# Kernel optimization log

Measured on AMD Instinct MI355X. Metric: run time of the kernel, lower is better.

Reference implementation:

```python
import jax, jax.numpy as jnp
import numpy as np

LAMBDA_SOFTMAX = 10.0  # opt.lambda_softmax
LEAKY_SLOPE = 0.1


def l2norm(x, axis):
    # matches torch F.normalize(p=2, eps=1e-12)
    n = jnp.linalg.norm(x, axis=axis, keepdims=True)
    return x / jnp.clip(n, 1e-12)


def setup_inputs() -> dict:
    key = jax.random.key(0)
    k1, k2, k3, k4, k5 = jax.random.split(key, 5)
    I, Q, T, S, D = 64, 49, 64, 64, 256  # n_img, n_region, n_txt, max_words, feature_size
    return {
        "local_img_query": jax.random.normal(k1, (I, Q, D), jnp.float32),
        "local_img_value": jax.random.normal(k2, (I, Q, D), jnp.float32),
        "local_text_key": jax.random.normal(k3, (T, S, D), jnp.float32),
        "local_text_value": jax.random.normal(k4, (T, S, D), jnp.float32),
        "text_length": jax.random.randint(k5, (T,), 8, S + 1, jnp.int32),
    }


def reference(local_img_query, local_img_value, local_text_key, local_text_value, text_length):
    # Vectorized form of the per-sentence Python loop in compute_i2t_sim.
    # Variable sentence lengths are handled with a mask over the padded word axis,
    # which reproduces the ragged torch math exactly (see comments).
    T, S, D = local_text_key.shape
    I, Q, _ = local_img_query.shape

    qn = l2norm(local_img_query, -1)   # [I,Q,D]
    kn = l2norm(local_text_key, -1)    # [T,S,D]

    # bmm(txt_key_norm, queryT): (B,S,D)x(B,D,Q) -> here [T,I,S,Q]
    attn = jnp.einsum('tsd,iqd->tisq', kn, qn)
    attn = jnp.where(attn > 0, attn, LEAKY_SLOPE * attn)      # LeakyReLU(0.1)
    # l2norm(attn, 2) normalizes over queryL per (t,i,s) row -> independent of padding
    attn = l2norm(attn, -1)
    attn = jnp.swapaxes(attn, 2, 3)                            # [T,I,Q,S]

    mask = jnp.arange(S)[None, :] < text_length[:, None]       # [T,S]
    logits = jnp.where(mask[:, None, None, :], attn * LAMBDA_SOFTMAX, -jnp.inf)
    attn = jax.nn.softmax(logits, axis=-1)                     # padded words -> exactly 0

    # focal_equal with sourceL = actual n_word of each sentence
    n_word = text_length.astype(attn.dtype)[:, None, None, None]
    funcF = attn * n_word - jnp.sum(attn, axis=-1, keepdims=True)
    fattn = (funcF > 0).astype(attn.dtype)                     # padded attn=0 -> funcF<0 -> 0
    tmp = fattn * attn
    attn = tmp / jnp.sum(tmp, axis=-1, keepdims=True)

    # bmm(valueT, attnT) -> weighted text context per (txt, img): [T,I,Q,D]
    wei = jnp.einsum('tsd,tiqs->tiqd', local_text_value, attn)
    wei = l2norm(wei, -1)

    # cosine similarity with image values along d, then mean over regions
    v = local_img_value[None]                                  # [1,I,Q,D]
    w12 = jnp.sum(v * wei, -1)
    denom = jnp.linalg.norm(v, axis=-1) * jnp.linalg.norm(wei, axis=-1)
    sim = w12 / jnp.clip(denom, 1e-8)                          # [T,I,Q]
    i2t = sim.mean(axis=-1)                                    # [T,I]
    return i2t.T                                               # [n_img, n_txt]
```

## Files before the change

kernel.cpp:

```cpp
#include <hip/hip_runtime.h>
#include <math.h>

#define I_N 64
#define Q_N 49
#define T_N 64
#define S_N 64
#define D_N 256

typedef __attribute__((ext_vector_type(8))) short short8;
typedef __attribute__((ext_vector_type(4))) float f32x4;
typedef unsigned short ushort_t;

__device__ __forceinline__ float waveReduceSum64(float v) {
    v += __shfl_xor(v, 1);
    v += __shfl_xor(v, 2);
    v += __shfl_xor(v, 4);
    v += __shfl_xor(v, 8);
    v += __shfl_xor(v, 16);
    v += __shfl_xor(v, 32);
    return v;
}

__device__ __forceinline__ ushort_t f2bf(float x) {
    unsigned u = __builtin_bit_cast(unsigned, x);
    unsigned r = (u + 0x7fffu + ((u >> 16) & 1u)) >> 16;
    return (ushort_t)r;
}
__device__ __forceinline__ float bf2f(ushort_t h) {
    unsigned u = ((unsigned)h) << 16;
    return __builtin_bit_cast(float, u);
}
__device__ __forceinline__ void split_bf16(float x, ushort_t& h, ushort_t& l) {
    h = f2bf(x);
    l = f2bf(x - bf2f(h));
}

__global__ void prep_norm(const float* __restrict__ q_in, const float* __restrict__ v_in,
                          const float* __restrict__ k_in,
                          ushort_t* __restrict__ qfh, ushort_t* __restrict__ qfl,
                          ushort_t* __restrict__ kfh, ushort_t* __restrict__ kfl,
                          float* __restrict__ vnorm) {
    int b = blockIdx.x;
    int tid = threadIdx.x;
    int isimg = (b < 4096) ? 1 : 0;
    int row = isimg ? b : (b - 4096);
    int hi = row >> 6, lo = row & 63;
    float x = 0.0f, vv = 0.0f;
    if (isimg) {
        if (lo < Q_N) {
            size_t base = ((size_t)hi * Q_N + lo) * D_N + tid;
            x = q_in[base];
            vv = v_in[base];
        }
    } else {
        x = k_in[(size_t)row * D_N + tid];
    }
    __shared__ float ws[8];
    float s1 = waveReduceSum64(x * x);
    float s2 = waveReduceSum64(vv * vv);
    int wv = tid >> 6, ln = tid & 63;
    if (ln == 0) { ws[wv] = s1; ws[4 + wv] = s2; }
    __syncthreads();
    float n1 = sqrtf(ws[0] + ws[1] + ws[2] + ws[3]);
    float xn = x / fmaxf(n1, 1e-12f);
    ushort_t h, l;
    split_bf16(xn, h, l);
    size_t off = ((size_t)hi << 14) + (size_t)((((lo >> 4) * 8 + (tid >> 5))) << 9)
               + (size_t)(((((tid >> 3) & 3) * 16 + (lo & 15))) << 3) + (tid & 7);
    if (isimg) {
        qfh[off] = h;
        qfl[off] = l;
        if (tid == 0) vnorm[row] = sqrtf(ws[4] + ws[5] + ws[6] + ws[7]);
    } else {
        kfh[off] = h;
        kfl[off] = l;
    }
}

__global__ void prep_vt(const float* __restrict__ tv,
                        ushort_t* __restrict__ vfh, ushort_t* __restrict__ vfl) {
    __shared__ float tile[64][65];
    int t = blockIdx.x;
    int d0 = blockIdx.y * 64;
    int tid = threadIdx.x;
    const float* src = tv + ((size_t)t << 14) + d0;
    ushort_t* dh = vfh + ((size_t)t << 14);
    ushort_t* dl = vfl + ((size_t)t << 14);
#pragma unroll
    for (int r = 0; r < 16; ++r) {
        int idx = r * 256 + tid;
        int s = idx >> 6, d = idx & 63;
        tile[s][d] = src[s * D_N + d];
    }
    __syncthreads();
#pragma unroll
    for (int r = 0; r < 16; ++r) {
        int idx = r * 256 + tid;
        int d = idx >> 6, s = idx & 63;
        int dg = d0 + d;
        float x = tile[s][d];
        ushort_t h, l;
        split_bf16(x, h, l);
        int dgrp = dg >> 4, lrd = dg & 15;
        int k0g = s >> 5, lk3 = (s >> 3) & 3, e = s & 7;
        size_t off = (size_t)(dgrp << 10) + (k0g << 9) + ((lk3 * 16 + lrd) << 3) + e;
        dh[off] = h;
        dl[off] = l;
    }
}

__global__ void prep_vp(const float* __restrict__ vimg, float* __restrict__ vP) {
    int i = blockIdx.x;
    int tid = threadIdx.x;
    const float* src = vimg + (size_t)i * Q_N * D_N;
    int wv = tid >> 6, lane = tid & 63;
    int lr = lane & 15, lk = lane >> 4;
    float* d0 = vP + ((size_t)i << 14) + (size_t)tid * 64;
#pragma unroll
    for (int nq = 0; nq < 4; ++nq) {
        int q = nq * 16 + lr;
#pragma unroll
        for (int md = 0; md < 4; ++md)
#pragma unroll
            for (int r = 0; r < 4; ++r) {
                int d = wv * 64 + md * 16 + lk * 4 + r;
                d0[nq * 16 + md * 4 + r] = (q < Q_N) ? src[q * D_N + d] : 0.0f;
            }
    }
}

__launch_bounds__(256, 4)
__global__ void i2t_mfma(const ushort_t* __restrict__ kfh, const ushort_t* __restrict__ kfl,
                         const ushort_t* __restrict__ qfh, const ushort_t* __restrict__ qfl,
                         const ushort_t* __restrict__ vfh, const ushort_t* __restrict__ vfl,
                         const float* __restrict__ vP,
                         const float* __restrict__ vnorm,
                         const int* __restrict__ tlen,
                         float* __restrict__ out)
{
    __shared__ __align__(16) unsigned char RK[33280];

    const int bid = blockIdx.x;
    const int xcd = bid & 7;
    const int j = bid >> 3;
    const int t = (xcd << 3) | (j & 7);
    const int i = j >> 3;

    const int tid = threadIdx.x;
    const int lane = tid & 63;
    const int w = tid >> 6;
    const int lr = lane & 15;
    const int lk = lane >> 4;

    const int wsr = (w >> 1) * 32;
    const int wq  = (w & 1) * 32;
    f32x4 acc[2][2];
#pragma unroll
    for (int a = 0; a < 2; ++a)
#pragma unroll
        for (int b = 0; b < 2; ++b) acc[a][b] = (f32x4){0.f, 0.f, 0.f, 0.f};
    {
        const ushort_t* kH = kfh + ((size_t)t << 14) + (size_t)(w >> 1) * 8192;
        const ushort_t* kL = kfl + ((size_t)t << 14) + (size_t)(w >> 1) * 8192;
        const ushort_t* qH = qfh + ((size_t)i << 14) + (size_t)(w & 1) * 8192;
        const ushort_t* qL = qfl + ((size_t)i << 14) + (size_t)(w & 1) * 8192;
#pragma unroll
        for (int k8 = 0; k8 < 8; ++k8) {
            int fo = k8 * 512 + lane * 8;
            short8 aH0 = *(const short8*)(kH + fo);
            short8 aL0 = *(const short8*)(kL + fo);
            short8 aH1 = *(const short8*)(kH + 4096 + fo);
            short8 aL1 = *(const short8*)(kL + 4096 + fo);
            short8 bH0 = *(const short8*)(qH + fo);
            short8 bL0 = *(const short8*)(qL + fo);
            short8 bH1 = *(const short8*)(qH + 4096 + fo);
            short8 bL1 = *(const short8*)(qL + 4096 + fo);
            acc[0][0] = __builtin_amdgcn_mfma_f32_16x16x32_bf16(aH0, bH0, acc[0][0], 0, 0, 0);
            acc[0][1] = __builtin_amdgcn_mfma_f32_16x16x32_bf16(aH0, bH1, acc[0][1], 0, 0, 0);
            acc[1][0] = __builtin_amdgcn_mfma_f32_16x16x32_bf16(aH1, bH0, acc[1][0], 0, 0, 0);
            acc[1][1] = __builtin_amdgcn_mfma_f32_16x16x32_bf16(aH1, bH1, acc[1][1], 0, 0, 0);
            acc[0][0] = __builtin_amdgcn_mfma_f32_16x16x32_bf16(aH0, bL0, acc[0][0], 0, 0, 0);
            acc[0][1] = __builtin_amdgcn_mfma_f32_16x16x32_bf16(aH0, bL1, acc[0][1], 0, 0, 0);
            acc[1][0] = __builtin_amdgcn_mfma_f32_16x16x32_bf16(aH1, bL0, acc[1][0], 0, 0, 0);
            acc[1][1] = __builtin_amdgcn_mfma_f32_16x16x32_bf16(aH1, bL1, acc[1][1], 0, 0, 0);
            acc[0][0] = __builtin_amdgcn_mfma_f32_16x16x32_bf16(aL0, bH0, acc[0][0], 0, 0, 0);
            acc[0][1] = __builtin_amdgcn_mfma_f32_16x16x32_bf16(aL0, bH1, acc[0][1], 0, 0, 0);
            acc[1][0] = __builtin_amdgcn_mfma_f32_16x16x32_bf16(aL1, bH0, acc[1][0], 0, 0, 0);
            acc[1][1] = __builtin_amdgcn_mfma_f32_16x16x32_bf16(aL1, bH1, acc[1][1], 0, 0, 0);
        }
    }
    {
        float* As = (float*)RK;
#pragma unroll
        for (int si = 0; si < 2; ++si)
#pragma unroll
            for (int qi = 0; qi < 2; ++qi)
#pragma unroll
                for (int r = 0; r < 4; ++r) {
                    int s = wsr + si * 16 + lk * 4 + r;
                    int q = wq + qi * 16 + lr;
                    float v = acc[si][qi][r];
                    v = (v > 0.0f) ? v : 0.1f * v;
                    As[s * 65 + q] = v;
                }
    }
    __syncthreads();

    {
        const float* As = (const float*)RK;
        float* rinv = (float*)(RK + 16640);
        int s = tid >> 2, part = tid & 3;
        float ss = 0.0f;
#pragma unroll
        for (int q0 = 0; q0 < 64; q0 += 4) {
            float v = As[s * 65 + q0 + part];
            ss += v * v;
        }
        ss += __shfl_xor(ss, 1);
        ss += __shfl_xor(ss, 2);
        if (part == 0) rinv[s] = 1.0f / fmaxf(sqrtf(ss), 1e-12f);
    }
    __syncthreads();

    const int len = tlen[t];
    {
        const float* As = (const float*)RK;
        const float* rinv = (const float*)(RK + 16640);
        ushort_t* Ph = (ushort_t*)(RK + 16896);
        ushort_t* Pl = (ushort_t*)(RK + 25088);
        const float thr = 1.0f / (float)len;
        int q = tid >> 2, part = tid & 3;
        float logit[16];
        float m = -INFINITY;
#pragma unroll
        for (int k = 0; k < 16; ++k) {
            int s = part * 16 + k;
            float lg = (s < len) ? 10.0f * As[s * 65 + q] * rinv[s] : -INFINITY;
            logit[k] = lg;
            m = fmaxf(m, lg);
        }
        m = fmaxf(m, __shfl_xor(m, 1));
        m = fmaxf(m, __shfl_xor(m, 2));
        float p[16];
        float sum = 0.0f;
#pragma unroll
        for (int k = 0; k < 16; ++k) {
            int s = part * 16 + k;
            float e = (s < len) ? __expf(logit[k] - m) : 0.0f;
            p[k] = e;
            sum += e;
        }
        sum += __shfl_xor(sum, 1);
        sum += __shfl_xor(sum, 2);
        float inv = 1.0f / sum;
        float sk = 0.0f;
#pragma unroll
        for (int k = 0; k < 16; ++k) {
            p[k] *= inv;
            if (p[k] > thr) sk += p[k];
        }
        sk += __shfl_xor(sk, 1);
        sk += __shfl_xor(sk, 2);
        float iv2 = 1.0f / sk;

        ushort_t hh[16], ll[16];
#pragma unroll
        for (int k = 0; k < 16; ++k) {
            float pv = (p[k] > thr) ? p[k] * iv2 : 0.0f;
            if (q >= Q_N) pv = 0.0f;
            split_bf16(pv, hh[k], ll[k]);
        }
        int c0 = (2 * part) ^ (q & 7);
        int c1 = (2 * part + 1) ^ (q & 7);
        short8 v0, v1;
#pragma unroll
        for (int k = 0; k < 8; ++k) { v0[k] = (short)hh[k]; v1[k] = (short)hh[k + 8]; }
        *(short8*)(Ph + q * 64 + (c0 << 3)) = v0;
        *(short8*)(Ph + q * 64 + (c1 << 3)) = v1;
#pragma unroll
        for (int k = 0; k < 8; ++k) { v0[k] = (short)ll[k]; v1[k] = (short)ll[k + 8]; }
        *(short8*)(Pl + q * 64 + (c0 << 3)) = v0;
        *(short8*)(Pl + q * 64 + (c1 << 3)) = v1;
    }
    __syncthreads();

    f32x4 acc2[4][4];
#pragma unroll
    for (int a = 0; a < 4; ++a)
#pragma unroll
        for (int b = 0; b < 4; ++b) acc2[a][b] = (f32x4){0.f, 0.f, 0.f, 0.f};
    {
        const ushort_t* vH = vfh + ((size_t)t << 14) + (size_t)w * 4096;
        const ushort_t* vL = vfl + ((size_t)t << 14) + (size_t)w * 4096;
        const ushort_t* PH = (const ushort_t*)(RK + 16896);
        const ushort_t* PL = (const ushort_t*)(RK + 25088);
#pragma unroll
        for (int k0g = 0; k0g < 2; ++k0g) {
#pragma unroll
            for (int md = 0; md < 4; ++md) {
                int vo = md * 1024 + k0g * 512 + lane * 8;
                short8 vh = *(const short8*)(vH + vo);
                short8 vl = *(const short8*)(vL + vo);
#pragma unroll
                for (int nq = 0; nq < 4; ++nq) {
                    int qrow = nq * 16 + lr;
                    int o = qrow * 64 + (((k0g * 4 + lk) ^ (qrow & 7)) << 3);
                    short8 ph = *(const short8*)(PH + o);
                    short8 pl = *(const short8*)(PL + o);
                    acc2[md][nq] = __builtin_amdgcn_mfma_f32_16x16x32_bf16(vh, ph, acc2[md][nq], 0, 0, 0);
                    acc2[md][nq] = __builtin_amdgcn_mfma_f32_16x16x32_bf16(vl, ph, acc2[md][nq], 0, 0, 0);
                    acc2[md][nq] = __builtin_amdgcn_mfma_f32_16x16x32_bf16(vh, pl, acc2[md][nq], 0, 0, 0);
                }
            }
        }
    }

    {
        float* wsq = (float*)RK;
        float* wdv = (float*)(RK + 1024);
        const float* vPb = vP + ((((size_t)i * 4 + w) * 64 + lane) << 6);
#pragma unroll
        for (int nq = 0; nq < 4; ++nq) {
            float s2 = 0.0f, dv = 0.0f;
#pragma unroll
            for (int md = 0; md < 4; ++md) {
                f32x4 vv = *(const f32x4*)(vPb + nq * 16 + md * 4);
#pragma unroll
                for (int r = 0; r < 4; ++r) {
                    float wv = acc2[md][nq][r];
                    s2 += wv * wv;
                    dv += wv * vv[r];
                }
            }
            s2 += __shfl_xor(s2, 16);
            s2 += __shfl_xor(s2, 32);
            dv += __shfl_xor(dv, 16);
            dv += __shfl_xor(dv, 32);
            if (lane < 16) {
                wsq[w * 64 + nq * 16 + lane] = s2;
                wdv[w * 64 + nq * 16 + lane] = dv;
            }
        }
    }
    __syncthreads();
    if (tid < 64) {
        const float* wsq = (const float*)RK;
        const float* wdv = (const float*)(RK + 1024);
        int q = tid;
        float s2 = 0.0f, dv = 0.0f;
#pragma unroll
        for (int ww = 0; ww < 4; ++ww) {
            s2 += wsq[ww * 64 + q];
            dv += wdv[ww * 64 + q];
        }
        float sim = 0.0f;
        if (q < Q_N) {
            float wn = sqrtf(s2);
            float w12 = dv / fmaxf(wn, 1e-12f);
            float wnn = wn / fmaxf(wn, 1e-12f);
            float denom = fmaxf(vnorm[i * 64 + q] * wnn, 1e-8f);
            sim = w12 / denom;
        }
        sim = waveReduceSum64(sim);
        if (tid == 0) out[(size_t)i * T_N + t] = sim * (1.0f / (float)Q_N);
    }
}

extern "C" void kernel_launch(void* const* d_in, const int* in_sizes, int n_in,
                              void* d_out, int out_size, void* d_ws, size_t ws_size,
                              hipStream_t stream) {
    const float* img_query = (const float*)d_in[0];
    const float* img_value = (const float*)d_in[1];
    const float* text_key  = (const float*)d_in[2];
    const float* text_val  = (const float*)d_in[3];
    const int*   text_len  = (const int*)d_in[4];
    float* out = (float*)d_out;

    const size_t NPAD = (size_t)64 * 64 * 256;
    ushort_t* qfh = (ushort_t*)d_ws;
    ushort_t* qfl = qfh + NPAD;
    ushort_t* kfh = qfl + NPAD;
    ushort_t* kfl = kfh + NPAD;
    ushort_t* vfh = kfl + NPAD;
    ushort_t* vfl = vfh + NPAD;
    float* vnorm  = (float*)(vfl + NPAD);
    float* vP     = vnorm + I_N * 64;

    prep_norm<<<8192, 256, 0, stream>>>(img_query, img_value, text_key,
                                        qfh, qfl, kfh, kfl, vnorm);
    prep_vt<<<dim3(T_N, 4), 256, 0, stream>>>(text_val, vfh, vfl);
    prep_vp<<<I_N, 256, 0, stream>>>(img_value, vP);

    i2t_mfma<<<T_N * I_N, 256, 0, stream>>>(kfh, kfl, qfh, qfl, vfh, vfl,
                                            vP, vnorm, text_len, out);
}
```

Measured before the change: 112.2 us.

## Merge prep kernels into one launch and split second GEMM into two passes

The three preprocessing kernels are merged into a single launch that dispatches on block index, which removes two kernel launches and the gaps between them. The second MFMA stage in the main kernel now runs as two passes over half of the D tiles, folding each pass's accumulators straight into the norm and dot-product partial sums. This halves the live accumulator registers (from 16 f32x4 to 8), which may ease register pressure and allow the launch-bounds occupancy of 4 blocks without spilling. The merged prep kernel always reserves the 64x65 shared tile for every block, which could lower occupancy for the normalization blocks.

```diff
diff --git a/kernel.cpp b/kernel.cpp
--- a/kernel.cpp
+++ b/kernel.cpp
@@ -35,97 +35,95 @@
     l = f2bf(x - bf2f(h));
 }
 
-__global__ void prep_norm(const float* __restrict__ q_in, const float* __restrict__ v_in,
-                          const float* __restrict__ k_in,
-                          ushort_t* __restrict__ qfh, ushort_t* __restrict__ qfl,
-                          ushort_t* __restrict__ kfh, ushort_t* __restrict__ kfl,
-                          float* __restrict__ vnorm) {
+__global__ void prep_all(const float* __restrict__ q_in, const float* __restrict__ v_in,
+                         const float* __restrict__ k_in, const float* __restrict__ tv,
+                         ushort_t* __restrict__ qfh, ushort_t* __restrict__ qfl,
+                         ushort_t* __restrict__ kfh, ushort_t* __restrict__ kfl,
+                         ushort_t* __restrict__ vfh, ushort_t* __restrict__ vfl,
+                         float* __restrict__ vP, float* __restrict__ vnorm) {
+    __shared__ float tile[64][65];
+    __shared__ float ws[8];
     int b = blockIdx.x;
     int tid = threadIdx.x;
-    int isimg = (b < 4096) ? 1 : 0;
-    int row = isimg ? b : (b - 4096);
-    int hi = row >> 6, lo = row & 63;
-    float x = 0.0f, vv = 0.0f;
-    if (isimg) {
-        if (lo < Q_N) {
-            size_t base = ((size_t)hi * Q_N + lo) * D_N + tid;
-            x = q_in[base];
-            vv = v_in[base];
+
+    if (b < 8192) {
+        int isimg = (b < 4096) ? 1 : 0;
+        int row = isimg ? b : (b - 4096);
+        int hi = row >> 6, lo = row & 63;
+        float x = 0.0f, vv = 0.0f;
+        if (isimg) {
+            if (lo < Q_N) {
+                size_t base = ((size_t)hi * Q_N + lo) * D_N + tid;
+                x = q_in[base];
+                vv = v_in[base];
+            }
+        } else {
+            x = k_in[(size_t)row * D_N + tid];
+        }
+        float s1 = waveReduceSum64(x * x);
+        float s2 = waveReduceSum64(vv * vv);
+        int wv = tid >> 6, ln = tid & 63;
+        if (ln == 0) { ws[wv] = s1; ws[4 + wv] = s2; }
+        __syncthreads();
+        float n1 = sqrtf(ws[0] + ws[1] + ws[2] + ws[3]);
+        float xn = x / fmaxf(n1, 1e-12f);
+        ushort_t h, l;
+        split_bf16(xn, h, l);
+        size_t off = ((size_t)hi << 14) + (size_t)((((lo >> 4) * 8 + (tid >> 5))) << 9)
+                   + (size_t)(((((tid >> 3) & 3) * 16 + (lo & 15))) << 3) + (tid & 7);
+        if (isimg) {
+            qfh[off] = h;
+            qfl[off] = l;
+            if (tid == 0) vnorm[row] = sqrtf(ws[4] + ws[5] + ws[6] + ws[7]);
+        } else {
+            kfh[off] = h;
+            kfl[off] = l;
+        }
+    } else if (b < 8448) {
+        int bb = b - 8192;
+        int t = bb >> 2;
+        int d0 = (bb & 3) * 64;
+        const float* src = tv + ((size_t)t << 14) + d0;
+        ushort_t* dh = vfh + ((size_t)t << 14);
+        ushort_t* dl = vfl + ((size_t)t << 14);
+#pragma unroll
+        for (int r = 0; r < 16; ++r) {
+            int idx = r * 256 + tid;
+            int s = idx >> 6, d = idx & 63;
+            tile[s][d] = src[s * D_N + d];
+        }
+        __syncthreads();
+#pragma unroll
+        for (int r = 0; r < 16; ++r) {
+            int idx = r * 256 + tid;
+            int d = idx >> 6, s = idx & 63;
+            int dg = d0 + d;
+            float x = tile[s][d];
+            ushort_t h, l;
+            split_bf16(x, h, l);
+            int dgrp = dg >> 4, lrd = dg & 15;
+            int k0g = s >> 5, lk3 = (s >> 3) & 3, e = s & 7;
+            size_t off = (size_t)(dgrp << 10) + (k0g << 9) + ((lk3 * 16 + lrd) << 3) + e;
+            dh[off] = h;
+            dl[off] = l;
         }
     } else {
-        x = k_in[(size_t)row * D_N + tid];
-    }
-    __shared__ float ws[8];
-    float s1 = waveReduceSum64(x * x);
-    float s2 = waveReduceSum64(vv * vv);
-    int wv = tid >> 6, ln = tid & 63;
-    if (ln == 0) { ws[wv] = s1; ws[4 + wv] = s2; }
-    __syncthreads();
-    float n1 = sqrtf(ws[0] + ws[1] + ws[2] + ws[3]);
-    float xn = x / fmaxf(n1, 1e-12f);
-    ushort_t h, l;
-    split_bf16(xn, h, l);
-    size_t off = ((size_t)hi << 14) + (size_t)((((lo >> 4) * 8 + (tid >> 5))) << 9)
-               + (size_t)(((((tid >> 3) & 3) * 16 + (lo & 15))) << 3) + (tid & 7);
-    if (isimg) {
-        qfh[off] = h;
-        qfl[off] = l;
-        if (tid == 0) vnorm[row] = sqrtf(ws[4] + ws[5] + ws[6] + ws[7]);
-    } else {
-        kfh[off] = h;
-        kfl[off] = l;
-    }
-}
-
-__global__ void prep_vt(const float* __restrict__ tv,
-                        ushort_t* __restrict__ vfh, ushort_t* __restrict__ vfl) {
-    __shared__ float tile[64][65];
-    int t = blockIdx.x;
-    int d0 = blockIdx.y * 64;
-    int tid = threadIdx.x;
-    const float* src = tv + ((size_t)t << 14) + d0;
-    ushort_t* dh = vfh + ((size_t)t << 14);
-    ushort_t* dl = vfl + ((size_t)t << 14);
-#pragma unroll
-    for (int r = 0; r < 16; ++r) {
-        int idx = r * 256 + tid;
-        int s = idx >> 6, d = idx & 63;
-        tile[s][d] = src[s * D_N + d];
-    }
-    __syncthreads();
-#pragma unroll
-    for (int r = 0; r < 16; ++r) {
-        int idx = r * 256 + tid;
-        int d = idx >> 6, s = idx & 63;
-        int dg = d0 + d;
-        float x = tile[s][d];
-        ushort_t h, l;
-        split_bf16(x, h, l);
-        int dgrp = dg >> 4, lrd = dg & 15;
-        int k0g = s >> 5, lk3 = (s >> 3) & 3, e = s & 7;
-        size_t off = (size_t)(dgrp << 10) + (k0g << 9) + ((lk3 * 16 + lrd) << 3) + e;
-        dh[off] = h;
-        dl[off] = l;
-    }
-}
-
-__global__ void prep_vp(const float* __restrict__ vimg, float* __restrict__ vP) {
-    int i = blockIdx.x;
-    int tid = threadIdx.x;
-    const float* src = vimg + (size_t)i * Q_N * D_N;
-    int wv = tid >> 6, lane = tid & 63;
-    int lr = lane & 15, lk = lane >> 4;
-    float* d0 = vP + ((size_t)i << 14) + (size_t)tid * 64;
-#pragma unroll
-    for (int nq = 0; nq < 4; ++nq) {
-        int q = nq * 16 + lr;
-#pragma unroll
-        for (int md = 0; md < 4; ++md)
-#pragma unroll
-            for (int r = 0; r < 4; ++r) {
-                int d = wv * 64 + md * 16 + lk * 4 + r;
-                d0[nq * 16 + md * 4 + r] = (q < Q_N) ? src[q * D_N + d] : 0.0f;
-            }
+        int i = b - 8448;
+        const float* src = v_in + (size_t)i * Q_N * D_N;
+        int wv = tid >> 6, lane = tid & 63;
+        int lr = lane & 15, lk = lane >> 4;
+        float* d0 = vP + ((size_t)i << 14) + (size_t)tid * 64;
+#pragma unroll
+        for (int nq = 0; nq < 4; ++nq) {
+            int q = nq * 16 + lr;
+#pragma unroll
+            for (int md = 0; md < 4; ++md)
+#pragma unroll
+                for (int r = 0; r < 4; ++r) {
+                    int d = wv * 64 + md * 16 + lk * 4 + r;
+                    d0[nq * 16 + md * 4 + r] = (q < Q_N) ? src[q * D_N + d] : 0.0f;
+                }
+        }
     }
 }
 
@@ -158,7 +156,7 @@
 #pragma unroll
     for (int a = 0; a < 2; ++a)
 #pragma unroll
-        for (int b = 0; b < 2; ++b) acc[a][b] = (f32x4){0.f, 0.f, 0.f, 0.f};
+        for (int b2 = 0; b2 < 2; ++b2) acc[a][b2] = (f32x4){0.f, 0.f, 0.f, 0.f};
     {
         const ushort_t* kH = kfh + ((size_t)t << 14) + (size_t)(w >> 1) * 8192;
         const ushort_t* kL = kfl + ((size_t)t << 14) + (size_t)(w >> 1) * 8192;
@@ -284,54 +282,63 @@
     }
     __syncthreads();
 
-    f32x4 acc2[4][4];
-#pragma unroll
-    for (int a = 0; a < 4; ++a)
-#pragma unroll
-        for (int b = 0; b < 4; ++b) acc2[a][b] = (f32x4){0.f, 0.f, 0.f, 0.f};
+    float s2a[4] = {0.f, 0.f, 0.f, 0.f}, dva[4] = {0.f, 0.f, 0.f, 0.f};
     {
         const ushort_t* vH = vfh + ((size_t)t << 14) + (size_t)w * 4096;
         const ushort_t* vL = vfl + ((size_t)t << 14) + (size_t)w * 4096;
         const ushort_t* PH = (const ushort_t*)(RK + 16896);
         const ushort_t* PL = (const ushort_t*)(RK + 25088);
-#pragma unroll
-        for (int k0g = 0; k0g < 2; ++k0g) {
-#pragma unroll
-            for (int md = 0; md < 4; ++md) {
-                int vo = md * 1024 + k0g * 512 + lane * 8;
-                short8 vh = *(const short8*)(vH + vo);
-                short8 vl = *(const short8*)(vL + vo);
-#pragma unroll
-                for (int nq = 0; nq < 4; ++nq) {
-                    int qrow = nq * 16 + lr;
-                    int o = qrow * 64 + (((k0g * 4 + lk) ^ (qrow & 7)) << 3);
-                    short8 ph = *(const short8*)(PH + o);
-                    short8 pl = *(const short8*)(PL + o);
-                    acc2[md][nq] = __builtin_amdgcn_mfma_f32_16x16x32_bf16(vh, ph, acc2[md][nq], 0, 0, 0);
-                    acc2[md][nq] = __builtin_amdgcn_mfma_f32_16x16x32_bf16(vl, ph, acc2[md][nq], 0, 0, 0);
-                    acc2[md][nq] = __builtin_amdgcn_mfma_f32_16x16x32_bf16(vh, pl, acc2[md][nq], 0, 0, 0);
+        const float* vPb = vP + ((((size_t)i * 4 + w) * 64 + lane) << 6);
+#pragma unroll
+        for (int pass = 0; pass < 2; ++pass) {
+            f32x4 acc2[2][4];
+#pragma unroll
+            for (int a = 0; a < 2; ++a)
+#pragma unroll
+                for (int b2 = 0; b2 < 4; ++b2) acc2[a][b2] = (f32x4){0.f, 0.f, 0.f, 0.f};
+#pragma unroll
+            for (int k0g = 0; k0g < 2; ++k0g) {
+#pragma unroll
+                for (int mdq = 0; mdq < 2; ++mdq) {
+                    int md = pass * 2 + mdq;
+                    int vo = md * 1024 + k0g * 512 + lane * 8;
+                    short8 vh = *(const short8*)(vH + vo);
+                    short8 vl = *(const short8*)(vL + vo);
+#pragma unroll
+                    for (int nq = 0; nq < 4; ++nq) {
+                        int qrow = nq * 16 + lr;
+                        int o = qrow * 64 + (((k0g * 4 + lk) ^ (qrow & 7)) << 3);
+                        short8 ph = *(const short8*)(PH + o);
+                        short8 pl = *(const short8*)(PL + o);
+                        acc2[mdq][nq] = __builtin_amdgcn_mfma_f32_16x16x32_bf16(vh, ph, acc2[mdq][nq], 0, 0, 0);
+                        acc2[mdq][nq] = __builtin_amdgcn_mfma_f32_16x16x32_bf16(vl, ph, acc2[mdq][nq], 0, 0, 0);
+                        acc2[mdq][nq] = __builtin_amdgcn_mfma_f32_16x16x32_bf16(vh, pl, acc2[mdq][nq], 0, 0, 0);
+                    }
                 }
             }
+#pragma unroll
+            for (int nq = 0; nq < 4; ++nq) {
+#pragma unroll
+                for (int mdq = 0; mdq < 2; ++mdq) {
+                    int md = pass * 2 + mdq;
+                    f32x4 vv = *(const f32x4*)(vPb + nq * 16 + md * 4);
+#pragma unroll
+                    for (int r = 0; r < 4; ++r) {
+                        float wv = acc2[mdq][nq][r];
+                        s2a[nq] += wv * wv;
+                        dva[nq] += wv * vv[r];
+                    }
+                }
+            }
         }
     }
 
     {
         float* wsq = (float*)RK;
         float* wdv = (float*)(RK + 1024);
-        const float* vPb = vP + ((((size_t)i * 4 + w) * 64 + lane) << 6);
 #pragma unroll
         for (int nq = 0; nq < 4; ++nq) {
-            float s2 = 0.0f, dv = 0.0f;
-#pragma unroll
-            for (int md = 0; md < 4; ++md) {
-                f32x4 vv = *(const f32x4*)(vPb + nq * 16 + md * 4);
-#pragma unroll
-                for (int r = 0; r < 4; ++r) {
-                    float wv = acc2[md][nq][r];
-                    s2 += wv * wv;
-                    dv += wv * vv[r];
-                }
-            }
+            float s2 = s2a[nq], dv = dva[nq];
             s2 += __shfl_xor(s2, 16);
             s2 += __shfl_xor(s2, 32);
             dv += __shfl_xor(dv, 16);
@@ -386,10 +393,8 @@
     float* vnorm  = (float*)(vfl + NPAD);
     float* vP     = vnorm + I_N * 64;
 
-    prep_norm<<<8192, 256, 0, stream>>>(img_query, img_value, text_key,
-                                        qfh, qfl, kfh, kfl, vnorm);
-    prep_vt<<<dim3(T_N, 4), 256, 0, stream>>>(text_val, vfh, vfl);
-    prep_vp<<<I_N, 256, 0, stream>>>(img_value, vP);
+    prep_all<<<8512, 256, 0, stream>>>(img_query, img_value, text_key, text_val,
+                                       qfh, qfl, kfh, kfl, vfh, vfl, vP, vnorm);
 
     i2t_mfma<<<T_N * I_N, 256, 0, stream>>>(kfh, kfl, qfh, qfl, vfh, vfl,
                                             vP, vnorm, text_len, out);
```

New measurement: 126.1 us. 12.4% more time.
